# Kernel tuning notes

Hardware: AMD Instinct MI355X
Metric: run time of the kernel (lower is better)

## Reference

```python
import jax, jax.numpy as jnp
import numpy as np

N = 50000      # nodes
E = 800000     # edges (before self-loops)
HD = 256       # hidden_dim
H = 4          # heads
C = 64         # per-head channels (hidden_dim // 4)
L = 3          # num_layers
G = 512        # graphs in batch
NEG = 0.2      # LeakyReLU negative slope
EPS = 1e-5     # BatchNorm eps


def setup_inputs() -> dict:
    key = jax.random.key(0)
    ks = jax.random.split(key, 16)
    s_in = 1.0 / np.sqrt(HD)
    inp = {
        "x": jax.random.normal(ks[0], (N, 9), dtype=jnp.float32),
        "edge_index": jax.random.randint(ks[1], (2, E), 0, N, dtype=jnp.int64),
        "edge_attr": jax.random.normal(ks[2], (E, 5), dtype=jnp.float32),
        "batch": jnp.sort(jax.random.randint(ks[3], (N,), 0, G, dtype=jnp.int64)),
        # embeddings
        "Wn": jax.random.normal(ks[4], (9, HD), dtype=jnp.float32) / 3.0,
        "bn_b": jnp.zeros((HD,), jnp.float32),
        "We": jax.random.normal(ks[5], (5, HD), dtype=jnp.float32) / 2.3,
        "be_b": jnp.zeros((HD,), jnp.float32),
        # per-layer GATConv params (stacked over L)
        "lin_w": jax.random.normal(ks[6], (L, HD, H * C), dtype=jnp.float32) * s_in,
        "att_src": jax.random.normal(ks[7], (L, H, C), dtype=jnp.float32) * s_in,
        "att_dst": jax.random.normal(ks[8], (L, H, C), dtype=jnp.float32) * s_in,
        "lin_edge_w": jax.random.normal(ks[9], (L, HD, H * C), dtype=jnp.float32) * s_in,
        "att_edge": jax.random.normal(ks[10], (L, H, C), dtype=jnp.float32) * s_in,
        "conv_bias": jnp.zeros((L, H * C), jnp.float32),
        # BatchNorm affine params (eval mode: running_mean=0, running_var=1)
        "gamma": jnp.ones((L, HD), jnp.float32),
        "beta": jnp.zeros((L, HD), jnp.float32),
    }
    return inp


def _segment_softmax(logits, seg, num):
    m = jax.ops.segment_max(logits, seg, num_segments=num)
    m = jnp.where(jnp.isfinite(m), m, 0.0)
    e = jnp.exp(logits - m[seg])
    s = jax.ops.segment_sum(e, seg, num_segments=num)
    return e / (s[seg] + 1e-16)


def _gat_layer(x, row, col, edge_attr, lin_w, att_s, att_d, lin_e_w, att_e, bias):
    # add self-loops; self-loop edge_attr = mean of incoming edge_attr (PyG fill_value='mean')
    deg = jax.ops.segment_sum(jnp.ones((row.shape[0],), x.dtype), col, num_segments=N)
    loop_attr = jax.ops.segment_sum(edge_attr, col, num_segments=N) / jnp.maximum(deg, 1.0)[:, None]
    sl = jnp.arange(N, dtype=row.dtype)
    r = jnp.concatenate([row, sl])
    c = jnp.concatenate([col, sl])
    ea = jnp.concatenate([edge_attr, loop_attr], axis=0)  # [E+N, HD]

    xh = (x @ lin_w).reshape(N, H, C)                     # [N,H,C]
    a_src = jnp.einsum('nhc,hc->nh', xh, att_s)           # [N,H]
    a_dst = jnp.einsum('nhc,hc->nh', xh, att_d)
    eh = (ea @ lin_e_w).reshape(-1, H, C)                 # [E+N,H,C]
    a_e = jnp.einsum('ehc,hc->eh', eh, att_e)

    alpha = a_src[r] + a_dst[c] + a_e                     # [E+N,H]
    alpha = jnp.where(alpha >= 0, alpha, NEG * alpha)     # leaky_relu
    alpha = _segment_softmax(alpha, c, N)

    msg = xh[r] * alpha[:, :, None]                       # gather + weight
    out = jax.ops.segment_sum(msg, c, num_segments=N)     # scatter-add
    return out.reshape(N, H * C) + bias


def reference(x, edge_index, edge_attr, batch, Wn, bn_b, We, be_b,
              lin_w, att_src, att_dst, lin_edge_w, att_edge, conv_bias,
              gamma, beta):
    row, col = edge_index[0], edge_index[1]
    h = x @ Wn + bn_b                     # node embedding [N,HD]
    ea = edge_attr @ We + be_b            # edge embedding [E,HD]
    inv_std = 1.0 / jnp.sqrt(1.0 + EPS)   # BN eval, running stats (0,1)
    for l in range(L):
        h = _gat_layer(h, row, col, ea, lin_w[l], att_src[l], att_dst[l],
                       lin_edge_w[l], att_edge[l], conv_bias[l])
        h = h * inv_std * gamma[l] + beta[l]
        h = jax.nn.relu(h)                # dropout = identity (eval)
    # global mean pool over graphs
    cnt = jax.ops.segment_sum(jnp.ones((N,), h.dtype), batch, num_segments=G)
    pooled = jax.ops.segment_sum(h, batch, num_segments=G) / jnp.maximum(cnt, 1.0)[:, None]
    return pooled
```

## Files before the change

kernel.cpp:

```cpp
#include <hip/hip_runtime.h>
#include <hip/hip_fp16.h>
#include <math.h>

#define HD 256
#define NHEAD 4
#define CH 64
#define NLAYER 3
#define NEG_SLOPE 0.2f

typedef __attribute__((ext_vector_type(8))) _Float16 half8;
typedef __attribute__((ext_vector_type(4))) _Float16 half4v;
typedef __attribute__((ext_vector_type(4))) float float4v;
typedef __attribute__((ext_vector_type(4))) unsigned uint4v;

__global__ __launch_bounds__(256) void embed_count_kernel(
    const float* __restrict__ x, const float* __restrict__ Wn,
    const float* __restrict__ bn_b, _Float16* __restrict__ h, int N,
    const int* __restrict__ col, int* __restrict__ deg, int E,
    int embedBlocks) {
  int tid = threadIdx.x;
  if ((int)blockIdx.x < embedBlocks) {
    int base = blockIdx.x * 8;
    __shared__ float xs[8][9];
    int nn = N - base;
    if (nn > 8) nn = 8;
    if (tid < nn * 9) xs[tid / 9][tid % 9] = x[(size_t)base * 9 + tid];
    __syncthreads();
    float b = bn_b[tid];
    for (int i = 0; i < nn; ++i) {
      float v = b;
#pragma unroll
      for (int k = 0; k < 9; ++k) v += xs[i][k] * Wn[k * HD + tid];
      h[(size_t)(base + i) * HD + tid] = (_Float16)v;
    }
  } else {
    int e = (blockIdx.x - embedBlocks) * 256 + tid;
    if (e < E) atomicAdd(&deg[col[e]], 1);
  }
}

__global__ __launch_bounds__(256) void wc_bfrag_kernel(
    const float* __restrict__ lin_edge_w, const float* __restrict__ att_edge,
    const float* __restrict__ We, const float* __restrict__ be_b,
    float* __restrict__ Wc, float* __restrict__ bc,
    const float* __restrict__ lin_w, _Float16* __restrict__ Bf_hi) {
  int tid = threadIdx.x;
  if (blockIdx.x < 12) {
    int lh = blockIdx.x;
    int l = lh >> 2, hh = lh & 3;
    __shared__ float weff[256];
    int j = tid;
    const float* lw = lin_edge_w + (size_t)l * HD * HD + (size_t)j * HD + hh * CH;
    const float* ae = att_edge + l * HD + hh * CH;
    float s = 0.f;
#pragma unroll 8
    for (int c = 0; c < CH; ++c) s += lw[c] * ae[c];
    weff[j] = s;
    __syncthreads();
    if (j < 5) {
      float acc = 0.f;
      for (int t = 0; t < 256; ++t) acc += We[j * HD + t] * weff[t];
      Wc[j * 12 + lh] = acc;
    } else if (j == 5) {
      float acc = 0.f;
      for (int t = 0; t < 256; ++t) acc += be_b[t] * weff[t];
      bc[lh] = acc;
    }
  } else {
    int bid = (blockIdx.x - 12) * 4 + (tid >> 6);
    int l = bid >> 7;
    int kt = (bid >> 4) & 7, ntg = bid & 15;
    int lane = tid & 63;
    const float* B = lin_w + (size_t)l * HD * HD;
    size_t base = ((size_t)bid * 64 + lane) * 8;
    int k0 = kt * 32 + (lane >> 4) * 8;
    int n = ((ntg >= 8) ? 128 : 0) + (lane & 15) * 8 + (ntg & 7);
#pragma unroll
    for (int j = 0; j < 8; ++j) {
      Bf_hi[base + j] = (_Float16)B[(size_t)(k0 + j) * HD + n];
    }
  }
}

__global__ __launch_bounds__(256) void tile_sums_kernel(
    const int* __restrict__ deg, int* __restrict__ tsum, int N) {
  __shared__ int red[256];
  int i = blockIdx.x * 256 + threadIdx.x;
  red[threadIdx.x] = (i < N) ? deg[i] : 0;
  __syncthreads();
  for (int off = 128; off > 0; off >>= 1) {
    if (threadIdx.x < off) red[threadIdx.x] += red[threadIdx.x + off];
    __syncthreads();
  }
  if (threadIdx.x == 0) tsum[blockIdx.x] = red[0];
}

__global__ __launch_bounds__(64) void scan_tsums_kernel(
    const int* __restrict__ tsum, int* __restrict__ toff, int T) {
  int lane = threadIdx.x;
  int carry = 0;
  for (int base = 0; base < T; base += 64) {
    int i = base + lane;
    int orig = (i < T) ? tsum[i] : 0;
    int v = orig;
#pragma unroll
    for (int off = 1; off < 64; off <<= 1) {
      int t = __shfl_up(v, off, 64);
      if (lane >= off) v += t;
    }
    if (i < T) toff[i] = carry + v - orig;
    carry += __shfl(v, 63, 64);
  }
}

__global__ __launch_bounds__(256) void scan_local_kernel(
    const int* __restrict__ deg, const int* __restrict__ toff,
    int* __restrict__ row_start, int N, int E) {
  __shared__ int buf[256];
  int i = blockIdx.x * 256 + threadIdx.x;
  int v = (i < N) ? deg[i] : 0;
  buf[threadIdx.x] = v;
  __syncthreads();
  for (int off = 1; off < 256; off <<= 1) {
    int t = (threadIdx.x >= off) ? buf[threadIdx.x - off] : 0;
    __syncthreads();
    buf[threadIdx.x] += t;
    __syncthreads();
  }
  if (i < N) row_start[i] = toff[blockIdx.x] + buf[threadIdx.x] - v;
  if (blockIdx.x == 0 && threadIdx.x == 0) row_start[N] = E;
}

__global__ __launch_bounds__(256) void scatter_csr_ae_kernel(
    const int* __restrict__ row, const int* __restrict__ col,
    const float* __restrict__ edge_attr, const int* __restrict__ row_start,
    int* __restrict__ cursor, const float* __restrict__ Wc,
    const float* __restrict__ bc, unsigned* __restrict__ ecsr, int E) {
  __shared__ float sWc[60];
  __shared__ float sbc[12];
  int t = threadIdx.x;
  if (t < 60) sWc[t] = Wc[t];
  if (t < 12) sbc[t] = bc[t];
  __syncthreads();
  int e = blockIdx.x * 256 + t;
  if (e >= E) return;
  int c = col[e];
  int p = atomicAdd(&cursor[c], 1);
  float ea[5];
#pragma unroll
  for (int k = 0; k < 5; ++k) ea[k] = edge_attr[(size_t)e * 5 + k];
  unsigned rec[8];
  rec[0] = (unsigned)row[e];
#pragma unroll
  for (int l = 0; l < NLAYER; ++l) {
    float av[NHEAD];
#pragma unroll
    for (int hh = 0; hh < NHEAD; ++hh) {
      int lh = l * NHEAD + hh;
      float s = sbc[lh];
#pragma unroll
      for (int k = 0; k < 5; ++k) s += ea[k] * sWc[k * 12 + lh];
      av[hh] = s;
    }
    __half2 p0 = __floats2half2_rn(av[0], av[1]);
    __half2 p1 = __floats2half2_rn(av[2], av[3]);
    rec[1 + 2 * l] = *(unsigned*)&p0;
    rec[2 + 2 * l] = *(unsigned*)&p1;
  }
  rec[7] = 0u;
  int slot = row_start[c] + p;
  uint4v* dst = (uint4v*)(ecsr + (size_t)slot * 8);
  uint4v v0 = {rec[0], rec[1], rec[2], rec[3]};
  uint4v v1 = {rec[4], rec[5], rec[6], rec[7]};
  dst[0] = v0;
  dst[1] = v1;
}

__global__ __launch_bounds__(512) void mfma_gemm_fused_kernel(
    const _Float16* __restrict__ A, const _Float16* __restrict__ Bf_hi,
    const float* __restrict__ att_s, const float* __restrict__ att_d,
    __half* __restrict__ xh_h, float* __restrict__ a_src,
    float* __restrict__ a_dst, int N) {
  __shared__ _Float16 sBh[4096];
  const int tid = threadIdx.x;
  const int wave = tid >> 6, lane = tid & 63;
  const int m = lane & 15, quad = lane >> 4;
  const int y = blockIdx.y;
  const int rowbase = blockIdx.x * 128 + wave * 16;
  const int arow = rowbase + m;
  const int arowc = (arow < N) ? arow : (N - 1);

  float4v acc[8];
#pragma unroll
  for (int nt = 0; nt < 8; ++nt) acc[nt] = (float4v){0.f, 0.f, 0.f, 0.f};

  for (int kt = 0; kt < 8; ++kt) {
    __syncthreads();
    {
      const float4* gh = (const float4*)(Bf_hi + ((size_t)kt * 16 + y * 8) * 512);
      ((float4*)sBh)[tid] = gh[tid];
    }
    half8 a = *(const half8*)(A + (size_t)arowc * HD + kt * 32 + quad * 8);
    __syncthreads();
#pragma unroll
    for (int nt = 0; nt < 8; ++nt) {
      half8 bhi = *(const half8*)&sBh[nt * 512 + lane * 8];
      acc[nt] = __builtin_amdgcn_mfma_f32_16x16x32_f16(a, bhi, acc[nt], 0, 0, 0);
    }
  }

  const int hh = y * 2 + (m >> 3);
  const int colbase = y * 128 + m * 8;
  float ats[8], atd[8];
#pragma unroll
  for (int nt = 0; nt < 8; ++nt) {
    ats[nt] = att_s[colbase + nt];
    atd[nt] = att_d[colbase + nt];
  }
  _Float16* xf = (_Float16*)xh_h;
#pragma unroll
  for (int r = 0; r < 4; ++r) {
    int orow = rowbase + quad * 4 + r;
    bool valid = orow < N;
    float ps = 0.f, pd = 0.f;
    half8 h0;
#pragma unroll
    for (int nt = 0; nt < 8; ++nt) {
      h0[nt] = (_Float16)acc[nt][r];
      ps += acc[nt][r] * ats[nt];
      pd += acc[nt][r] * atd[nt];
    }
    if (valid) {
      *(half8*)(xf + (size_t)orow * HD + colbase) = h0;
    }
    ps += __shfl_xor(ps, 1, 64);
    ps += __shfl_xor(ps, 2, 64);
    ps += __shfl_xor(ps, 4, 64);
    pd += __shfl_xor(pd, 1, 64);
    pd += __shfl_xor(pd, 2, 64);
    pd += __shfl_xor(pd, 4, 64);
    if (valid && (m & 7) == 0) {
      a_src[(size_t)orow * NHEAD + hh] = ps;
      a_dst[(size_t)orow * NHEAD + hh] = pd;
    }
  }
}

__global__ __launch_bounds__(256) void fused_aggregate_kernel(
    const __half* __restrict__ xh_h, const unsigned* __restrict__ ecsr,
    const int* __restrict__ row_start, int lsel,
    const float* __restrict__ a_src, const float* __restrict__ a_dst,
    const float* __restrict__ cb, const float* __restrict__ gm,
    const float* __restrict__ bt, float inv_std, _Float16* __restrict__ hout,
    int N) {
  const int tid = threadIdx.x;
  const int lane = tid & 63;
  const int wave = tid >> 6;
  const int halfw = lane >> 5;
  const int l32 = lane & 31;
  const int hw = l32 >> 3;
  const int eu = l32 & 7;
  const int chb = l32 * 8;
  const char* __restrict__ xb = (const char*)xh_h;
  const char* __restrict__ eb = (const char*)ecsr;
  const char* __restrict__ ab = (const char*)a_src;
  const int aofs = 1 + 2 * lsel + (hw >> 1);
  const bool hi_half = (hw & 1);
  const int bsrc = lane & 32;
  const int bw = lane & 56;

  int n = blockIdx.x * 8 + wave * 2 + halfw;
  bool valid = n < N;
  int nc = valid ? n : (N - 1);

  int s = row_start[nc];
  int e = row_start[nc + 1];
  if (!valid) e = s;

  half8 sv = *(const half8*)(xb + ((unsigned)nc << 9) + ((unsigned)l32 << 4));
  float based = a_dst[(size_t)nc * 4 + hw];

  float acc[8];
#pragma unroll
  for (int k = 0; k < 8; ++k) acc[k] = 0.f;
  float zpart = 0.f, aepart = 0.f;

  for (int chunk = s; chunk < e; chunk += 8) {
    int myedge = chunk + eu;
    bool mev = myedge < e;
    unsigned r_w = 0, aw = 0;
    if (mev) {
      const unsigned* rp = (const unsigned*)(eb + ((size_t)(unsigned)myedge << 5));
      r_w = rp[0];
      aw = rp[aofs];
    }
    unsigned ru[8];
#pragma unroll
    for (int u = 0; u < 8; ++u) ru[u] = (unsigned)__shfl((int)r_w, bsrc + u, 64);
    half8 xr[8];
#pragma unroll
    for (int u = 0; u < 8; ++u)
      xr[u] = *(const half8*)(xb + (size_t)((ru[u] << 9) + ((unsigned)l32 << 4)));

    float w_my = 0.f, ae = 0.f;
    if (mev) {
      __half2 h2 = *(__half2*)&aw;
      ae = hi_half ? __high2float(h2) : __low2float(h2);
      float lg = *(const float*)(ab + ((unsigned)r_w << 4) + ((unsigned)hw << 2))
                 + based + ae;
      lg = (lg >= 0.f) ? lg : NEG_SLOPE * lg;
      w_my = __expf(lg);
    }
    zpart += w_my;
    aepart += ae;

#pragma unroll
    for (int u = 0; u < 8; ++u) {
      float w = __shfl(w_my, bw + u, 64);
#pragma unroll
      for (int k = 0; k < 8; ++k) acc[k] += w * (float)xr[u][k];
    }
  }
  zpart += __shfl_xor(zpart, 1, 64);
  zpart += __shfl_xor(zpart, 2, 64);
  zpart += __shfl_xor(zpart, 4, 64);
  aepart += __shfl_xor(aepart, 1, 64);
  aepart += __shfl_xor(aepart, 2, 64);
  aepart += __shfl_xor(aepart, 4, 64);

  float dinv = (e > s) ? 1.0f / (float)(e - s) : 1.0f;
  float sl = *(const float*)(ab + ((unsigned)nc << 4) + ((unsigned)hw << 2))
             + based + aepart * dinv;
  sl = (sl >= 0.f) ? sl : NEG_SLOPE * sl;
  float wself = __expf(sl);
#pragma unroll
  for (int k = 0; k < 8; ++k) acc[k] += wself * (float)sv[k];
  float zinv = 1.0f / (zpart + wself + 1e-16f);

  if (valid) {
    half8 ho;
#pragma unroll
    for (int k = 0; k < 8; ++k) {
      float gsk = gm[chb + k] * inv_std;
      float ofk = cb[chb + k] * gsk + bt[chb + k];
      ho[k] = (_Float16)fmaxf(acc[k] * zinv * gsk + ofk, 0.f);
    }
    *(half8*)&hout[(size_t)n * HD + chb] = ho;
  }
}

__global__ __launch_bounds__(128) void pool_kernel(
    const _Float16* __restrict__ h, const int* __restrict__ batch,
    float* __restrict__ out, int N) {
  int g = blockIdx.x;
  int tid = threadIdx.x;
  __shared__ int s_lo, s_hi;
  if (tid == 0) {
    int lo = 0, hi = N;
    while (lo < hi) { int mid = (lo + hi) >> 1; if (batch[mid] < g) lo = mid + 1; else hi = mid; }
    s_lo = lo;
    lo = 0; hi = N;
    while (lo < hi) { int mid = (lo + hi) >> 1; if (batch[mid] < g + 1) lo = mid + 1; else hi = mid; }
    s_hi = lo;
  }
  __syncthreads();
  int lo = s_lo, hi = s_hi;
  const __half2* h2 = (const __half2*)h;
  float a0 = 0.f, b0 = 0.f, a1 = 0.f, b1 = 0.f;
  float a2 = 0.f, b2 = 0.f, a3 = 0.f, b3 = 0.f;
  int n = lo;
  for (; n + 4 <= hi; n += 4) {
    __half2 v0 = h2[(size_t)(n + 0) * 128 + tid];
    __half2 v1 = h2[(size_t)(n + 1) * 128 + tid];
    __half2 v2 = h2[(size_t)(n + 2) * 128 + tid];
    __half2 v3 = h2[(size_t)(n + 3) * 128 + tid];
    a0 += __low2float(v0); b0 += __high2float(v0);
    a1 += __low2float(v1); b1 += __high2float(v1);
    a2 += __low2float(v2); b2 += __high2float(v2);
    a3 += __low2float(v3); b3 += __high2float(v3);
  }
  for (; n < hi; ++n) {
    __half2 v = h2[(size_t)n * 128 + tid];
    a0 += __low2float(v); b0 += __high2float(v);
  }
  float sa = (a0 + a1) + (a2 + a3);
  float sb = (b0 + b1) + (b2 + b3);
  int cnt = hi - lo;
  float inv = 1.0f / (float)(cnt > 0 ? cnt : 1);
  float2 o;
  o.x = sa * inv;
  o.y = sb * inv;
  *(float2*)&out[(size_t)g * HD + tid * 2] = o;
}

extern "C" void kernel_launch(void* const* d_in, const int* in_sizes, int n_in,
                              void* d_out, int out_size, void* d_ws, size_t ws_size,
                              hipStream_t stream) {
  const float* x = (const float*)d_in[0];
  const int* ei = (const int*)d_in[1];
  const float* edge_attr = (const float*)d_in[2];
  const int* batch = (const int*)d_in[3];
  const float* Wn = (const float*)d_in[4];
  const float* bn_b = (const float*)d_in[5];
  const float* We = (const float*)d_in[6];
  const float* be_b = (const float*)d_in[7];
  const float* lin_w = (const float*)d_in[8];
  const float* att_src = (const float*)d_in[9];
  const float* att_dst = (const float*)d_in[10];
  const float* lin_edge_w = (const float*)d_in[11];
  const float* att_edge = (const float*)d_in[12];
  const float* conv_bias = (const float*)d_in[13];
  const float* gamma = (const float*)d_in[14];
  const float* beta = (const float*)d_in[15];

  const int N = in_sizes[3];
  const int E = in_sizes[1] / 2;
  const int G = out_size / HD;
  const int* row = ei;
  const int* col = ei + E;

  char* ws = (char*)d_ws;
  size_t off = 0;
  auto alloc = [&](size_t bytes) -> char* {
    char* p = ws + off;
    off += (bytes + 255) & ~(size_t)255;
    return p;
  };
  _Float16* h = (_Float16*)alloc((size_t)N * HD * 2);
  __half* xh_h = (__half*)alloc((size_t)N * HD * 2);
  float* a_src = (float*)alloc((size_t)N * NHEAD * 4);
  float* a_dst = (float*)alloc((size_t)N * NHEAD * 4);
  unsigned* ecsr = (unsigned*)alloc((size_t)E * 32);
  int* deg = (int*)alloc((size_t)N * 4);
  int* row_start = (int*)alloc((size_t)(N + 1) * 4);
  int* cursor = (int*)alloc((size_t)N * 4);
  int* tsum = (int*)alloc(4096);
  int* toff = (int*)alloc(4096);
  float* Wc = (float*)alloc(64 * 4);
  float* bc = (float*)alloc(16 * 4);
  _Float16* Bf_hi = (_Float16*)alloc((size_t)NLAYER * HD * HD * 2);

  (void)hipMemsetAsync(deg, 0, (size_t)N * 4, stream);
  (void)hipMemsetAsync(cursor, 0, (size_t)N * 4, stream);

  int embedBlocks = (N + 7) / 8;
  int countBlocks = (E + 255) / 256;
  embed_count_kernel<<<embedBlocks + countBlocks, 256, 0, stream>>>(
      x, Wn, bn_b, h, N, col, deg, E, embedBlocks);
  wc_bfrag_kernel<<<12 + NLAYER * 32, 256, 0, stream>>>(
      lin_edge_w, att_edge, We, be_b, Wc, bc, lin_w, Bf_hi);
  int T = (N + 255) / 256;
  tile_sums_kernel<<<T, 256, 0, stream>>>(deg, tsum, N);
  scan_tsums_kernel<<<1, 64, 0, stream>>>(tsum, toff, T);
  scan_local_kernel<<<T, 256, 0, stream>>>(deg, toff, row_start, N, E);
  scatter_csr_ae_kernel<<<(E + 255) / 256, 256, 0, stream>>>(
      row, col, edge_attr, row_start, cursor, Wc, bc, ecsr, E);

  const float inv_std = 1.0f / sqrtf(1.0f + 1e-5f);
  for (int l = 0; l < NLAYER; ++l) {
    dim3 gg((N + 127) / 128, 2);
    mfma_gemm_fused_kernel<<<gg, 512, 0, stream>>>(
        h, Bf_hi + (size_t)l * HD * HD,
        att_src + l * HD, att_dst + l * HD, xh_h, a_src, a_dst, N);
    fused_aggregate_kernel<<<(N + 7) / 8, 256, 0, stream>>>(
        xh_h, ecsr, row_start, l, a_src, a_dst,
        conv_bias + l * HD, gamma + l * HD, beta + l * HD, inv_std, h, N);
  }
  pool_kernel<<<G, 128, 0, stream>>>(h, batch, (float*)d_out, N);
}
```

Baseline: 476.3 us.

## Software-pipeline edge gathers in aggregate kernel with double-buffered registers

Restructures the per-node edge loop in the aggregation kernel into a two-stage software pipeline. The next 8-edge chunk's CSR entries, neighbour features and source attention logits are loaded while the current chunk is consumed, which hides gather latency. Both half-waves now iterate to the shared max chunk count, and block size drops from 256 to 128 threads. The extra buffer roughly doubles live registers for the feature gathers, which may reduce occupancy.

Result: slower. 498.9 us (+4.7%).

```diff
diff --git a/kernel.cpp b/kernel.cpp
--- a/kernel.cpp
+++ b/kernel.cpp
@@ -246,7 +246,50 @@
   }
 }
 
-__global__ __launch_bounds__(256) void fused_aggregate_kernel(
+#define AGG_LOAD(IT, SUF)                                                      \
+  {                                                                            \
+    int myedge = s + ((IT) << 3) + eu;                                         \
+    mev##SUF = myedge < e;                                                     \
+    r##SUF = 0u;                                                               \
+    aw##SUF = 0u;                                                              \
+    if (mev##SUF) {                                                            \
+      const unsigned* rp =                                                     \
+          (const unsigned*)(eb + ((size_t)(unsigned)myedge << 5));             \
+      r##SUF = rp[0];                                                          \
+      aw##SUF = rp[aofs];                                                      \
+    }                                                                          \
+    _Pragma("unroll")                                                          \
+    for (int u = 0; u < 8; ++u) {                                              \
+      unsigned ruu = (unsigned)__shfl((int)r##SUF, bsrc + u, 64);              \
+      xr##SUF[u] = *(const half8*)(xb + (size_t)((ruu << 9) +                  \
+                                                 ((unsigned)l32 << 4)));       \
+    }                                                                          \
+    as##SUF = mev##SUF ? *(const float*)(ab + ((unsigned)r##SUF << 4) +        \
+                                         ((unsigned)hw << 2))                  \
+                       : 0.f;                                                  \
+  }
+
+#define AGG_CONSUME(SUF)                                                       \
+  {                                                                            \
+    float w = 0.f, ae = 0.f;                                                   \
+    if (mev##SUF) {                                                            \
+      __half2 h2 = *(__half2*)&aw##SUF;                                        \
+      ae = hi_half ? __high2float(h2) : __low2float(h2);                       \
+      float lg = as##SUF + based + ae;                                         \
+      lg = (lg >= 0.f) ? lg : NEG_SLOPE * lg;                                  \
+      w = __expf(lg);                                                          \
+    }                                                                          \
+    zpart += w;                                                                \
+    aepart += ae;                                                              \
+    _Pragma("unroll")                                                          \
+    for (int u = 0; u < 8; ++u) {                                              \
+      float wb = __shfl(w, bw + u, 64);                                        \
+      _Pragma("unroll")                                                        \
+      for (int k = 0; k < 8; ++k) acc[k] += wb * (float)xr##SUF[u][k];         \
+    }                                                                          \
+  }
+
+__global__ __launch_bounds__(128) void fused_aggregate_kernel(
     const __half* __restrict__ xh_h, const unsigned* __restrict__ ecsr,
     const int* __restrict__ row_start, int lsel,
     const float* __restrict__ a_src, const float* __restrict__ a_dst,
@@ -269,7 +312,7 @@
   const int bsrc = lane & 32;
   const int bw = lane & 56;
 
-  int n = blockIdx.x * 8 + wave * 2 + halfw;
+  int n = blockIdx.x * 4 + wave * 2 + halfw;
   bool valid = n < N;
   int nc = valid ? n : (N - 1);
 
@@ -285,42 +328,27 @@
   for (int k = 0; k < 8; ++k) acc[k] = 0.f;
   float zpart = 0.f, aepart = 0.f;
 
-  for (int chunk = s; chunk < e; chunk += 8) {
-    int myedge = chunk + eu;
-    bool mev = myedge < e;
-    unsigned r_w = 0, aw = 0;
-    if (mev) {
-      const unsigned* rp = (const unsigned*)(eb + ((size_t)(unsigned)myedge << 5));
-      r_w = rp[0];
-      aw = rp[aofs];
-    }
-    unsigned ru[8];
-#pragma unroll
-    for (int u = 0; u < 8; ++u) ru[u] = (unsigned)__shfl((int)r_w, bsrc + u, 64);
-    half8 xr[8];
-#pragma unroll
-    for (int u = 0; u < 8; ++u)
-      xr[u] = *(const half8*)(xb + (size_t)((ru[u] << 9) + ((unsigned)l32 << 4)));
-
-    float w_my = 0.f, ae = 0.f;
-    if (mev) {
-      __half2 h2 = *(__half2*)&aw;
-      ae = hi_half ? __high2float(h2) : __low2float(h2);
-      float lg = *(const float*)(ab + ((unsigned)r_w << 4) + ((unsigned)hw << 2))
-                 + based + ae;
-      lg = (lg >= 0.f) ? lg : NEG_SLOPE * lg;
-      w_my = __expf(lg);
-    }
-    zpart += w_my;
-    aepart += ae;
-
-#pragma unroll
-    for (int u = 0; u < 8; ++u) {
-      float w = __shfl(w_my, bw + u, 64);
-#pragma unroll
-      for (int k = 0; k < 8; ++k) acc[k] += w * (float)xr[u][k];
-    }
-  }
+  int nck = (e - s + 7) >> 3;
+  int other = __shfl_xor(nck, 32, 64);
+  int nmax = nck > other ? nck : other;
+
+  half8 xrA[8], xrB[8];
+  unsigned rA, rB, awA, awB;
+  float asA, asB;
+  bool mevA, mevB;
+
+  if (nmax > 0) {
+    AGG_LOAD(0, A)
+    int it = 0;
+    for (; it + 1 < nmax; it += 2) {
+      AGG_LOAD(it + 1, B)
+      AGG_CONSUME(A)
+      if (it + 2 < nmax) AGG_LOAD(it + 2, A)
+      AGG_CONSUME(B)
+    }
+    if (it < nmax) AGG_CONSUME(A)
+  }
+
   zpart += __shfl_xor(zpart, 1, 64);
   zpart += __shfl_xor(zpart, 2, 64);
   zpart += __shfl_xor(zpart, 4, 64);
@@ -462,7 +490,7 @@
     mfma_gemm_fused_kernel<<<gg, 512, 0, stream>>>(
         h, Bf_hi + (size_t)l * HD * HD,
         att_src + l * HD, att_dst + l * HD, xh_h, a_src, a_dst, N);
-    fused_aggregate_kernel<<<(N + 7) / 8, 256, 0, stream>>>(
+    fused_aggregate_kernel<<<(N + 3) / 4, 128, 0, stream>>>(
         xh_h, ecsr, row_start, l, a_src, a_dst,
         conv_bias + l * HD, gamma + l * HD, beta + l * HD, inv_std, h, N);
   }
```

## Split edge CSR records per layer and load them directly in aggregation

Applied to the files above, without the earlier changes.

The 32-byte edge record holding all layers is replaced by three 16-byte per-layer arrays, each holding the source row and that layer's four fp16 edge-attention terms. In the aggregate kernel every lane now loads all 8 edge records of a chunk itself with a 16-byte load, instead of one lane per edge loading and then broadcasting row ids and weights with shuffles. Each lane also computes all 8 exp weights and keeps its own softmax-denominator sums, so the final cross-lane reductions go away. This cuts the shuffles and the edge bytes read per layer, at the cost of redundant record loads and 8x redundant exp/logit work per lane, plus more scatter writes and workspace.

Result: no change. 483.6 us (+1.5%).

```diff
diff --git a/kernel.cpp b/kernel.cpp
--- a/kernel.cpp
+++ b/kernel.cpp
@@ -149,8 +149,9 @@
   float ea[5];
 #pragma unroll
   for (int k = 0; k < 5; ++k) ea[k] = edge_attr[(size_t)e * 5 + k];
-  unsigned rec[8];
-  rec[0] = (unsigned)row[e];
+  unsigned r0 = (unsigned)row[e];
+  int slot = row_start[c] + p;
+  size_t E4 = (size_t)E * 4;
 #pragma unroll
   for (int l = 0; l < NLAYER; ++l) {
     float av[NHEAD];
@@ -164,16 +165,9 @@
     }
     __half2 p0 = __floats2half2_rn(av[0], av[1]);
     __half2 p1 = __floats2half2_rn(av[2], av[3]);
-    rec[1 + 2 * l] = *(unsigned*)&p0;
-    rec[2 + 2 * l] = *(unsigned*)&p1;
-  }
-  rec[7] = 0u;
-  int slot = row_start[c] + p;
-  uint4v* dst = (uint4v*)(ecsr + (size_t)slot * 8);
-  uint4v v0 = {rec[0], rec[1], rec[2], rec[3]};
-  uint4v v1 = {rec[4], rec[5], rec[6], rec[7]};
-  dst[0] = v0;
-  dst[1] = v1;
+    uint4v v = {r0, *(unsigned*)&p0, *(unsigned*)&p1, 0u};
+    *(uint4v*)(ecsr + l * E4 + (size_t)slot * 4) = v;
+  }
 }
 
 __global__ __launch_bounds__(512) void mfma_gemm_fused_kernel(
@@ -247,8 +241,8 @@
 }
 
 __global__ __launch_bounds__(256) void fused_aggregate_kernel(
-    const __half* __restrict__ xh_h, const unsigned* __restrict__ ecsr,
-    const int* __restrict__ row_start, int lsel,
+    const __half* __restrict__ xh_h, const unsigned* __restrict__ elay,
+    const int* __restrict__ row_start,
     const float* __restrict__ a_src, const float* __restrict__ a_dst,
     const float* __restrict__ cb, const float* __restrict__ gm,
     const float* __restrict__ bt, float inv_std, _Float16* __restrict__ hout,
@@ -259,15 +253,12 @@
   const int halfw = lane >> 5;
   const int l32 = lane & 31;
   const int hw = l32 >> 3;
-  const int eu = l32 & 7;
   const int chb = l32 * 8;
   const char* __restrict__ xb = (const char*)xh_h;
-  const char* __restrict__ eb = (const char*)ecsr;
+  const char* __restrict__ eb = (const char*)elay;
   const char* __restrict__ ab = (const char*)a_src;
-  const int aofs = 1 + 2 * lsel + (hw >> 1);
   const bool hi_half = (hw & 1);
-  const int bsrc = lane & 32;
-  const int bw = lane & 56;
+  const int awsel = (hw >> 1);
 
   int n = blockIdx.x * 8 + wave * 2 + halfw;
   bool valid = n < N;
@@ -286,47 +277,47 @@
   float zpart = 0.f, aepart = 0.f;
 
   for (int chunk = s; chunk < e; chunk += 8) {
-    int myedge = chunk + eu;
-    bool mev = myedge < e;
-    unsigned r_w = 0, aw = 0;
-    if (mev) {
-      const unsigned* rp = (const unsigned*)(eb + ((size_t)(unsigned)myedge << 5));
-      r_w = rp[0];
-      aw = rp[aofs];
-    }
-    unsigned ru[8];
-#pragma unroll
-    for (int u = 0; u < 8; ++u) ru[u] = (unsigned)__shfl((int)r_w, bsrc + u, 64);
+    uint4v rc[8];
+#pragma unroll
+    for (int u = 0; u < 8; ++u) {
+      int ed = chunk + u;
+      ed = (ed < e) ? ed : (e - 1);
+      rc[u] = *(const uint4v*)(eb + ((size_t)(unsigned)ed << 4));
+    }
+    unsigned rows[8], aw[8];
+#pragma unroll
+    for (int u = 0; u < 8; ++u) {
+      rows[u] = rc[u][0];
+      aw[u] = awsel ? rc[u][2] : rc[u][1];
+    }
     half8 xr[8];
 #pragma unroll
     for (int u = 0; u < 8; ++u)
-      xr[u] = *(const half8*)(xb + (size_t)((ru[u] << 9) + ((unsigned)l32 << 4)));
-
-    float w_my = 0.f, ae = 0.f;
-    if (mev) {
-      __half2 h2 = *(__half2*)&aw;
-      ae = hi_half ? __high2float(h2) : __low2float(h2);
-      float lg = *(const float*)(ab + ((unsigned)r_w << 4) + ((unsigned)hw << 2))
-                 + based + ae;
+      xr[u] = *(const half8*)(xb + (((size_t)rows[u] << 9) +
+                                    ((unsigned)l32 << 4)));
+    float w[8];
+#pragma unroll
+    for (int u = 0; u < 8; ++u) {
+      __half2 h2 = *(__half2*)&aw[u];
+      float ae = hi_half ? __high2float(h2) : __low2float(h2);
+      float as_ = *(const float*)(ab + ((size_t)rows[u] << 4) +
+                                  ((unsigned)hw << 2));
+      float lg = as_ + based + ae;
       lg = (lg >= 0.f) ? lg : NEG_SLOPE * lg;
-      w_my = __expf(lg);
-    }
-    zpart += w_my;
-    aepart += ae;
-
+      float ww = __expf(lg);
+      bool mv = (chunk + u) < e;
+      ww = mv ? ww : 0.f;
+      ae = mv ? ae : 0.f;
+      zpart += ww;
+      aepart += ae;
+      w[u] = ww;
+    }
 #pragma unroll
     for (int u = 0; u < 8; ++u) {
-      float w = __shfl(w_my, bw + u, 64);
-#pragma unroll
-      for (int k = 0; k < 8; ++k) acc[k] += w * (float)xr[u][k];
-    }
-  }
-  zpart += __shfl_xor(zpart, 1, 64);
-  zpart += __shfl_xor(zpart, 2, 64);
-  zpart += __shfl_xor(zpart, 4, 64);
-  aepart += __shfl_xor(aepart, 1, 64);
-  aepart += __shfl_xor(aepart, 2, 64);
-  aepart += __shfl_xor(aepart, 4, 64);
+#pragma unroll
+      for (int k = 0; k < 8; ++k) acc[k] += w[u] * (float)xr[u][k];
+    }
+  }
 
   float dinv = (e > s) ? 1.0f / (float)(e - s) : 1.0f;
   float sl = *(const float*)(ab + ((unsigned)nc << 4) + ((unsigned)hw << 2))
@@ -430,7 +421,7 @@
   __half* xh_h = (__half*)alloc((size_t)N * HD * 2);
   float* a_src = (float*)alloc((size_t)N * NHEAD * 4);
   float* a_dst = (float*)alloc((size_t)N * NHEAD * 4);
-  unsigned* ecsr = (unsigned*)alloc((size_t)E * 32);
+  unsigned* ecsr = (unsigned*)alloc((size_t)E * 16 * NLAYER);
   int* deg = (int*)alloc((size_t)N * 4);
   int* row_start = (int*)alloc((size_t)(N + 1) * 4);
   int* cursor = (int*)alloc((size_t)N * 4);
@@ -463,7 +454,7 @@
         h, Bf_hi + (size_t)l * HD * HD,
         att_src + l * HD, att_dst + l * HD, xh_h, a_src, a_dst, N);
     fused_aggregate_kernel<<<(N + 7) / 8, 256, 0, stream>>>(
-        xh_h, ecsr, row_start, l, a_src, a_dst,
+        xh_h, ecsr + (size_t)l * E * 4, row_start, a_src, a_dst,
         conv_bias + l * HD, gamma + l * HD, beta + l * HD, inv_std, h, N);
   }
   pool_kernel<<<G, 128, 0, stream>>>(h, batch, (float*)d_out, N);
```
